# Optimization experiments

Measured on AMD Instinct MI355X. Metric: run time of the kernel, lower is better.

Reference implementation:

```python
import jax, jax.numpy as jnp
import numpy as np

NQ = 8          # n_qubits
NC = 4          # n_cycles of the angle encoder
PI = np.float32(np.pi)
LAYER_QUBITS = [[0, 1, 2, 3, 4, 5, 6, 7], [1, 3, 5, 7]]  # active qubits per conv layer
FINAL_QUBITS = [3, 7]                                    # active after last pooling
CX = jnp.array([[1, 0, 0, 0], [0, 1, 0, 0], [0, 0, 0, 1], [0, 0, 1, 0]], jnp.complex64)


def apply1(psi, U, q):
    """Apply 1-qubit gate U ((2,2) shared or (B,2,2) batched) on qubit q. psi: (B,2,...,2)."""
    psi = jnp.moveaxis(psi, 1 + q, -1)
    if U.ndim == 3:
        psi = jnp.einsum('bij,b...j->b...i', U, psi)
    else:
        psi = jnp.einsum('ij,...j->...i', U, psi)
    return jnp.moveaxis(psi, -1, 1 + q)


def apply2(psi, U, q0, q1):
    """Apply 2-qubit gate U (4,4) on (q0,q1); q0 is the more-significant wire."""
    psi = jnp.moveaxis(psi, (1 + q0, 1 + q1), (-2, -1))
    sh = psi.shape
    psi = jnp.einsum('ij,...j->...i', U, psi.reshape(sh[:-2] + (4,)))
    return jnp.moveaxis(psi.reshape(sh), (-2, -1), (1 + q0, 1 + q1))


def rz_mat(t):
    return jnp.array([[jnp.exp(-0.5j * t), 0.0], [0.0, jnp.exp(0.5j * t)]]).astype(jnp.complex64)


def ry_mat(t):
    c, s = jnp.cos(t / 2), jnp.sin(t / 2)
    return jnp.array([[c, -s], [s, c]]).astype(jnp.complex64)


def crx_mat(t):
    c = jnp.cos(t / 2).astype(jnp.complex64)
    s = jnp.sin(t / 2).astype(jnp.complex64)
    M = jnp.eye(4, dtype=jnp.complex64)
    return M.at[2, 2].set(c).at[3, 3].set(c).at[2, 3].set(-1j * s).at[3, 2].set(-1j * s)


def u3_mat(t, p, l):
    c, s = jnp.cos(t / 2), jnp.sin(t / 2)
    return jnp.array([[c + 0j, -jnp.exp(1j * l) * s],
                      [jnp.exp(1j * p) * s, jnp.exp(1j * (p + l)) * c]]).astype(jnp.complex64)


def expz(psi, q):
    """<Z_q> = P(q=0) - P(q=1)."""
    p = psi.real ** 2 + psi.imag ** 2
    p = jnp.moveaxis(p, 1 + q, 1).reshape(p.shape[0], 2, -1).sum(-1)
    return p[:, 0] - p[:, 1]


def encode(x):
    """Angle-encoding circuit (circuit_builder): NC cycles of RY(x) + CNOT ring."""
    B = x.shape[0]
    psi = jnp.zeros((B, 2 ** NQ), jnp.complex64).at[:, 0].set(1.0).reshape((B,) + (2,) * NQ)
    for c in range(NC):
        ang = x[:, c * NQ:(c + 1) * NQ]
        cc, ss = jnp.cos(ang / 2), jnp.sin(ang / 2)
        for q in range(NQ):
            U = jnp.stack([jnp.stack([cc[:, q], -ss[:, q]], -1),
                           jnp.stack([ss[:, q], cc[:, q]], -1)], -2).astype(jnp.complex64)
            psi = apply1(psi, U, q)
        for q in range(NQ):
            psi = apply2(psi, CX, q, (q + 1) % NQ)
    return psi


def forward(x, rz_p, ry_p, ry2_p, crx_p, u3_p, u3b_p, W1, b1, W2, b2):
    psi0 = encode(x)
    psi1 = psi0  # deepcopy of encoded state for the second feature map
    for layer in range(2):
        aq = LAYER_QUBITS[layer]
        n = len(aq)
        RZp, RYp, RY2p = rz_mat(rz_p[layer]), ry_mat(ry_p[layer]), ry_mat(ry2_p[layer])
        RZm, RZpl = rz_mat(-PI / 2), rz_mat(PI / 2)
        # circuit 1: ZNOTY-style conv blocks, even pairs then odd pairs
        for parity in (0, 1):
            for i in range(parity, n - 1, 2):
                qc, qt = aq[i], aq[i + 1]
                psi0 = apply1(psi0, RZm, qt)
                psi0 = apply2(psi0, CX, qt, qc)
                psi0 = apply1(psi0, RZp, qc)
                psi0 = apply1(psi0, RYp, qt)
                psi0 = apply2(psi0, CX, qc, qt)
                psi0 = apply1(psi0, RY2p, qt)
                psi0 = apply2(psi0, CX, qt, qc)
                psi0 = apply1(psi0, RZpl, qc)
        remain = [aq[i] for i in range(n) if i % 2 == 1]
        U3a = u3_mat(u3_p[layer, 0], u3_p[layer, 1], u3_p[layer, 2])
        for q in remain:
            psi0 = apply1(psi0, U3a, q)
        # circuit 2: CRX conv blocks, even pairs then odd pairs
        CRXp = crx_mat(crx_p[layer])
        for parity in (0, 1):
            for i in range(parity, n - 1, 2):
                psi1 = apply2(psi1, CRXp, aq[i], aq[i + 1])
        U3b = u3_mat(u3b_p[layer, 0], u3b_p[layer, 1], u3b_p[layer, 2])
        for q in remain:
            psi1 = apply1(psi1, U3b, q)
    xv = jnp.stack([expz(psi0, q) for q in FINAL_QUBITS], 1)  # (B,2)
    yv = jnp.stack([expz(psi1, q) for q in FINAL_QUBITS], 1)  # (B,2)
    feat = jnp.concatenate([xv, yv], 1)                       # (B,4)
    h = jnp.tanh(feat @ W1.T + b1)
    return jax.nn.sigmoid(h @ W2.T + b2)


def setup_inputs() -> dict:
    key = jax.random.key(0)
    ks = jax.random.split(key, 12)
    B = 8192
    return {
        'x': jax.random.normal(ks[0], (B, NC * NQ), jnp.float32),
        'rz_p': jax.random.normal(ks[1], (2,), jnp.float32) * 0.5,
        'ry_p': jax.random.normal(ks[2], (2,), jnp.float32) * 0.5,
        'ry2_p': jax.random.normal(ks[3], (2,), jnp.float32) * 0.5,
        'crx_p': jax.random.normal(ks[4], (2,), jnp.float32) * 0.5,
        'u3_p': jax.random.normal(ks[5], (2, 3), jnp.float32) * 0.5,
        'u3b_p': jax.random.normal(ks[6], (2, 3), jnp.float32) * 0.5,
        'W1': jax.random.normal(ks[7], (15, 4), jnp.float32) * 0.4,
        'b1': jax.random.normal(ks[8], (15,), jnp.float32) * 0.1,
        'W2': jax.random.normal(ks[9], (1, 15), jnp.float32) * 0.25,
        'b2': jax.random.normal(ks[10], (1,), jnp.float32) * 0.1,
    }


def reference(x, rz_p, ry_p, ry2_p, crx_p, u3_p, u3b_p, W1, b1, W2, b2):
    return forward(x, rz_p, ry_p, ry2_p, crx_p, u3_p, u3b_p, W1, b1, W2, b2)
```

## Files before the change

### kernel.cpp

```cpp
#include <hip/hip_runtime.h>

#define DEV __device__ __forceinline__


DEV int lpar(int lane, int m) { return __builtin_popcount(lane & m) & 1; }
constexpr int cpar(int v) { return (v ^ (v >> 1) ^ (v >> 2) ^ (v >> 3)) & 1; }

template<int LM, int SM, int LR, int SR>
DEV void ryr(float* p, float gc, float gs, int lane) {
  const float sg0 = lpar(lane, LR) ? gs : -gs;
  const float sg1 = -sg0;
  if constexpr (LM != 0) {
    float t[16];
    #pragma unroll
    for (int s = 0; s < 16; ++s) t[s] = __shfl_xor(p[s ^ SM], LM);
    #pragma unroll
    for (int s = 0; s < 16; ++s)
      p[s] = gc * p[s] + (cpar(s & SR) ? sg1 : sg0) * t[s];
  } else {
    constexpr int LOW = SM & (-SM);
    #pragma unroll
    for (int s = 0; s < 16; ++s) if (!(s & LOW)) {
      const int s1 = s ^ SM;
      float a = p[s], b = p[s1];
      float sg = cpar(s & SR) ? sg1 : sg0;
      p[s]  = gc * a + sg * b;
      p[s1] = gc * b - sg * a;
    }
  }
}

template<int LM, int SM, int LR, int SR>
DEV void u3_g(float* pr, float* pi, const float* u, int lane) {
  const bool hl = lpar(lane, LR);
  const float d0r = hl ? u[6] : u[0], d0i = hl ? u[7] : u[1];
  const float o0r = hl ? u[4] : u[2], o0i = hl ? u[5] : u[3];
  const float d1r = hl ? u[0] : u[6], d1i = hl ? u[1] : u[7];
  const float o1r = hl ? u[2] : u[4], o1i = hl ? u[3] : u[5];
  if constexpr (LM != 0) {
    float tr[16], ti[16];
    #pragma unroll
    for (int s = 0; s < 16; ++s) {
      tr[s] = __shfl_xor(pr[s ^ SM], LM);
      ti[s] = __shfl_xor(pi[s ^ SM], LM);
    }
    #pragma unroll
    for (int s = 0; s < 16; ++s) {
      const bool c1 = cpar(s & SR);
      const float dr = c1 ? d1r : d0r, di = c1 ? d1i : d0i;
      const float orr = c1 ? o1r : o0r, oi = c1 ? o1i : o0i;
      float ar = pr[s], ai = pi[s];
      pr[s] = dr*ar - di*ai + orr*tr[s] - oi*ti[s];
      pi[s] = dr*ai + di*ar + orr*ti[s] + oi*tr[s];
    }
  } else {
    constexpr int LOW = SM & (-SM);
    #pragma unroll
    for (int s = 0; s < 16; ++s) if (!(s & LOW)) {
      const int s1 = s ^ SM;
      const bool c1 = cpar(s & SR);
      const float dAr = c1 ? d1r : d0r, dAi = c1 ? d1i : d0i;
      const float oAr = c1 ? o1r : o0r, oAi = c1 ? o1i : o0i;
      const float dBr = c1 ? d0r : d1r, dBi = c1 ? d0i : d1i;
      const float oBr = c1 ? o0r : o1r, oBi = c1 ? o0i : o1i;
      float ar = pr[s], ai = pi[s], br = pr[s1], bi = pi[s1];
      pr[s]  = dAr*ar - dAi*ai + oAr*br - oAi*bi;
      pi[s]  = dAr*ai + dAi*ar + oAr*bi + oAi*br;
      pr[s1] = dBr*br - dBi*bi + oBr*ar - oBi*ai;
      pi[s1] = dBr*bi + dBi*br + oBr*ai + oBi*ar;
    }
  }
}

#define U4CLASS(Q)                                                            \
  if constexpr (!(((SRc == 0) && (Q & 2)) || ((SRt == 0) && (Q & 1)))) {      \
    const int r1 = R ^ Q, r2 = r1 ^ 2;                                        \
    const float2 wd = w2[r1 * 4 + r1],       wo = w2[r1 * 4 + (r1 ^ 1)];      \
    const float2 vd = w2[r2 * 4 + r1],       vo = w2[r2 * 4 + (r1 ^ 1)];      \
    _Pragma("unroll")                                                         \
    for (int s = 0; s < 16; ++s)                                              \
      if (((cpar(s & SRc) << 1) | cpar(s & SRt)) == Q) {                      \
        float ar = pr[s], ai = pi[s], br = tr[s], bi = ti[s];                 \
        pr[s] = wd.x*ar - wd.y*ai + wo.x*br - wo.y*bi;                        \
        pi[s] = wd.x*ai + wd.y*ar + wo.x*bi + wo.y*br;                        \
        tr[s] = vd.x*ar - vd.y*ai + vo.x*br - vo.y*bi;                        \
        ti[s] = vd.x*ai + vd.y*ar + vo.x*bi + vo.y*br;                        \
      }                                                                       \
  }

template<int LMc, int SMc, int LMt, int SMt, int LRc, int SRc, int LRt, int SRt>
DEV void u4_g(float* pr, float* pi, const float2* w2, int lane) {
  const int R = (lpar(lane, LRc) << 1) | lpar(lane, LRt);
  float tr[16], ti[16];
  #pragma unroll
  for (int s = 0; s < 16; ++s) {
    float vr = pr[s ^ SMt], vi = pi[s ^ SMt];
    if constexpr (LMt != 0) { vr = __shfl_xor(vr, LMt); vi = __shfl_xor(vi, LMt); }
    tr[s] = vr; ti[s] = vi;
  }
  U4CLASS(0) U4CLASS(1) U4CLASS(2) U4CLASS(3)
  #pragma unroll
  for (int s = 0; s < 16; ++s) {
    float br = tr[s ^ SMc], bi = ti[s ^ SMc];
    if constexpr (LMc != 0) { br = __shfl_xor(br, LMc); bi = __shfl_xor(bi, LMc); }
    pr[s] += br; pi[s] += bi;
  }
}

DEV void u3_make(float t, float p, float l, float* u) {
  float c = __cosf(0.5f * t), s = __sinf(0.5f * t);
  float cp = __cosf(p), sp = __sinf(p);
  float cl = __cosf(l), sl = __sinf(l);
  float cpl = __cosf(p + l), spl = __sinf(p + l);
  u[0] = c;        u[1] = 0.0f;
  u[2] = -cl * s;  u[3] = -sl * s;
  u[4] = cp * s;   u[5] = sp * s;
  u[6] = cpl * c;  u[7] = spl * c;
}

DEV void expz_fin(const float* pr, const float* pi, int lane, float& z3, float& z7) {
  float t3 = 0.0f, t7 = 0.0f;
  #pragma unroll
  for (int s = 0; s < 16; ++s) {
    float p = pr[s] * pr[s] + pi[s] * pi[s];
    t7 += p;
    t3 += (s & 1) ? -p : p;
  }
  if (lpar(lane, 10)) { t3 = -t3; t7 = -t7; }
  #pragma unroll
  for (int m = 1; m < 16; m <<= 1) {
    t3 += __shfl_xor(t3, m);
    t7 += __shfl_xor(t7, m);
  }
  z3 = t3; z7 = t7;
}


__global__ __launch_bounds__(256, 2)
void qcnn_kernel(const float* __restrict__ x,
                 const float* __restrict__ rz_p, const float* __restrict__ ry_p,
                 const float* __restrict__ ry2_p, const float* __restrict__ crx_p,
                 const float* __restrict__ u3_p, const float* __restrict__ u3b_p,
                 const float* __restrict__ W1, const float* __restrict__ b1,
                 const float* __restrict__ W2, const float* __restrict__ b2,
                 float* __restrict__ out, int B) {
  __shared__ __align__(8) float cw[128];

  const int tid  = threadIdx.x;
  const int lane = tid & 63;
  const int wave = tid >> 6;
  const int grp  = lane >> 4;
  const int sub  = lane & 15;
  const int st   = grp & 1;
  const int gb   = lane & 48;
  const int elem = blockIdx.x * 8 + wave * 2 + (grp >> 1);
  const int elemc = elem < B ? elem : (B - 1);

  if (tid < 32) {
    const int lay = tid >> 4, e = tid & 15, i4 = e >> 2, j4 = e & 3;
    const int base = tid & 48;
    const float c45 = 0.70710678118654752f;
    float rz = rz_p[lay], ry = ry_p[lay], ry2 = ry2_p[lay];
    float mr = (i4 == j4) ? c45 : 0.0f;
    float mi = (i4 == j4) ? ((i4 & 1) ? -c45 : c45) : 0.0f;
    { int t = (i4 & 1) ? (i4 ^ 2) : i4; int src = base | (t << 2) | j4;
      mr = __shfl(mr, src); mi = __shfl(mi, src); }
    { float cz = __cosf(0.5f * rz), sz = __sinf(0.5f * rz);
      float di = (i4 & 2) ? sz : -sz;
      float nr = cz * mr - di * mi, ni = cz * mi + di * mr; mr = nr; mi = ni; }
    { float cy = __cosf(0.5f * ry), sy = __sinf(0.5f * ry);
      int src = base | ((i4 ^ 1) << 2) | j4;
      float orr = __shfl(mr, src), oii = __shfl(mi, src);
      float sg = (i4 & 1) ? sy : -sy;
      mr = cy * mr + sg * orr; mi = cy * mi + sg * oii; }
    { int t = (i4 & 2) ? (i4 ^ 1) : i4; int src = base | (t << 2) | j4;
      mr = __shfl(mr, src); mi = __shfl(mi, src); }
    { float cy = __cosf(0.5f * ry2), sy = __sinf(0.5f * ry2);
      int src = base | ((i4 ^ 1) << 2) | j4;
      float orr = __shfl(mr, src), oii = __shfl(mi, src);
      float sg = (i4 & 1) ? sy : -sy;
      mr = cy * mr + sg * orr; mi = cy * mi + sg * oii; }
    { int t = (i4 & 1) ? (i4 ^ 2) : i4; int src = base | (t << 2) | j4;
      mr = __shfl(mr, src); mi = __shfl(mi, src); }
    { float di = (i4 & 2) ? c45 : -c45;
      float nr = c45 * mr - di * mi, ni = c45 * mi + di * mr; mr = nr; mi = ni; }
    cw[((lay * 2 + 0) * 16 + e) * 2]     = mr;
    cw[((lay * 2 + 0) * 16 + e) * 2 + 1] = mi;
  } else if (tid < 64) {
    const int t2 = tid - 32;
    const int lay = t2 >> 4, e = t2 & 15, i4 = e >> 2, j4 = e & 3;
    float t = crx_p[lay];
    float c = __cosf(0.5f * t), s = __sinf(0.5f * t);
    float mr = 0.0f, mi = 0.0f;
    if (i4 == j4) mr = (i4 < 2) ? 1.0f : c;
    if ((i4 >= 2) && ((i4 ^ j4) == 1)) mi = -s;
    cw[((lay * 2 + 1) * 16 + e) * 2]     = mr;
    cw[((lay * 2 + 1) * 16 + e) * 2 + 1] = mi;
  }

  float2 aa = ((const float2*)x)[(size_t)elemc * 16 + sub];
  float ch0 = __cosf(0.5f * aa.x), sh0 = __sinf(0.5f * aa.x);
  float ch1 = __cosf(0.5f * aa.y), sh1 = __sinf(0.5f * aa.y);

  float cq[8], sq[8];
  #pragma unroll
  for (int q = 0; q < 8; ++q) {
    cq[q] = __shfl((q & 1) ? ch1 : ch0, gb | (q >> 1));
    sq[q] = __shfl((q & 1) ? sh1 : sh0, gb | (q >> 1));
  }

  float p[16];
  {
    float g = ((sub & 8) ? sq[0] : cq[0]) * ((sub & 4) ? sq[2] : cq[2]) *
              ((sub & 2) ? sq[4] : cq[4]) * ((sub & 1) ? sq[6] : cq[6]);
    float h13[4] = {cq[1]*cq[3], cq[1]*sq[3], sq[1]*cq[3], sq[1]*sq[3]};
    float h57[4] = {cq[5]*cq[7], cq[5]*sq[7], sq[5]*cq[7], sq[5]*sq[7]};
    #pragma unroll
    for (int i = 0; i < 4; ++i) h13[i] *= g;
    #pragma unroll
    for (int s = 0; s < 16; ++s) p[s] = h13[s >> 2] * h57[s & 3];
  }

  #define ENC(k, LM, SM, LR, SR) {                                  \
    float gc = __shfl(((k) & 1) ? ch1 : ch0, gb | ((k) >> 1));      \
    float gs = __shfl(((k) & 1) ? sh1 : sh0, gb | ((k) >> 1));      \
    ryr<LM, SM, LR, SR>(p, gc, gs, lane); }

  ENC(8,  8,8, 7,15)  ENC(9,  4,8, 8,8)   ENC(10, 4,4, 12,8)  ENC(11, 2,4, 12,12)
  ENC(12, 2,2, 14,12) ENC(13, 1,2, 14,14) ENC(14, 1,1, 15,14) ENC(15, 8,9, 15,15)
  ENC(16, 12,0, 8,15) ENC(17, 0,12, 15,7) ENC(18, 6,0, 3,15)  ENC(19, 0,6, 15,3)
  ENC(20, 3,0, 1,15)  ENC(21, 0,3, 15,1)  ENC(22, 9,8, 0,15)  ENC(23, 4,9, 15,0)
  ENC(24, 12,12, 2,10) ENC(25, 6,12, 7,8) ENC(26, 6,6, 4,7)   ENC(27, 3,6, 11,4)
  ENC(28, 3,3, 10,11)  ENC(29, 9,11, 5,10) ENC(30, 13,1, 5,5) ENC(31, 8,5, 10,5)
  #undef ENC

  float pi_[16];
  #pragma unroll
  for (int s = 0; s < 16; ++s) pi_[s] = 0.0f;

  __syncthreads();
  const float2* w0 = ((const float2*)cw) + (0 * 2 + st) * 16;
  const float2* w1 = ((const float2*)cw) + (1 * 2 + st) * 16;

  u4_g<10,0,  0,10, 8,10, 5,2 >(p, pi_, w0, lane);
  u4_g<5,0,   0,5,  1,5,  10,1>(p, pi_, w0, lane);
  u4_g<10,8,  4,10, 0,10, 5,0 >(p, pi_, w0, lane);
  u4_g<5,4,   2,5,  0,5,  10,0>(p, pi_, w0, lane);
  u4_g<0,10,  5,0,  5,2,  1,5 >(p, pi_, w0, lane);
  u4_g<0,5,   10,8, 10,1, 0,10>(p, pi_, w0, lane);
  u4_g<4,10,  5,4,  5,0,  0,5 >(p, pi_, w0, lane);
  {
    float ua[8], ub[8], us[8];
    u3_make(u3_p[0], u3_p[1], u3_p[2], ua);
    u3_make(u3b_p[0], u3b_p[1], u3b_p[2], ub);
    #pragma unroll
    for (int k = 0; k < 8; ++k) us[k] = st ? ub[k] : ua[k];
    u3_g<0,10, 5,2 >(p, pi_, us, lane);
    u3_g<0,5,  10,1>(p, pi_, us, lane);
    u3_g<4,10, 5,0 >(p, pi_, us, lane);
    u3_g<2,5,  10,0>(p, pi_, us, lane);
  }
  u4_g<0,10,  0,5,  5,2,  10,1>(p, pi_, w1, lane);
  u4_g<4,10,  2,5,  5,0,  10,0>(p, pi_, w1, lane);
  u4_g<0,5,   4,10, 10,1, 5,0 >(p, pi_, w1, lane);
  {
    float ua[8], ub[8], us[8];
    u3_make(u3_p[3], u3_p[4], u3_p[5], ua);
    u3_make(u3b_p[3], u3b_p[4], u3b_p[5], ub);
    #pragma unroll
    for (int k = 0; k < 8; ++k) us[k] = st ? ub[k] : ua[k];
    u3_g<0,5,  10,1>(p, pi_, us, lane);
    u3_g<2,5,  10,0>(p, pi_, us, lane);
  }

  float z3, z7;
  expz_fin(p, pi_, lane, z3, z7);
  float o3 = __shfl_xor(z3, 16);
  float o7 = __shfl_xor(z7, 16);
  const float f0 = st ? o3 : z3, f1 = st ? o7 : z7;
  const float f2 = st ? z3 : o3, f3 = st ? z7 : o7;

  const int j = (sub < 15) ? sub : 0;
  float acc = W1[j * 4 + 0] * f0 + W1[j * 4 + 1] * f1 +
              W1[j * 4 + 2] * f2 + W1[j * 4 + 3] * f3 + b1[j];
  float e2 = __expf(2.0f * acc);
  float th = (e2 - 1.0f) / (e2 + 1.0f);
  float part = (sub < 15) ? th * W2[j] : 0.0f;
  #pragma unroll
  for (int m = 1; m < 16; m <<= 1) part += __shfl_xor(part, m);

  if (sub == 0 && st == 0 && elem < B) {
    float z = part + b2[0];
    out[elem] = 1.0f / (1.0f + __expf(-z));
  }
}

extern "C" void kernel_launch(void* const* d_in, const int* in_sizes, int n_in,
                              void* d_out, int out_size, void* d_ws, size_t ws_size,
                              hipStream_t stream) {
  (void)n_in; (void)out_size; (void)d_ws; (void)ws_size;
  const float* x     = (const float*)d_in[0];
  const float* rz_p  = (const float*)d_in[1];
  const float* ry_p  = (const float*)d_in[2];
  const float* ry2_p = (const float*)d_in[3];
  const float* crx_p = (const float*)d_in[4];
  const float* u3_p  = (const float*)d_in[5];
  const float* u3b_p = (const float*)d_in[6];
  const float* W1    = (const float*)d_in[7];
  const float* b1    = (const float*)d_in[8];
  const float* W2    = (const float*)d_in[9];
  const float* b2    = (const float*)d_in[10];
  float* out = (float*)d_out;

  const int B = in_sizes[0] / 32;
  const int blocks = (B + 7) / 8;
  qcnn_kernel<<<dim3(blocks), dim3(256), 0, stream>>>(
      x, rz_p, ry_p, ry2_p, crx_p, u3_p, u3b_p, W1, b1, W2, b2, out, B);
}
```

Measured before the change: 136.4 us.

## Remap state to 32 lanes x 8 amplitudes, run two branches sequentially

Before, each batch element used 32 lanes (two 16-lane halves, one per circuit branch), each holding 16 amplitudes. Now each element uses 32 lanes holding 8 amplitudes each. The encoded state is computed once and the two conv branches run one after another in a loop that reuses it. This halves per-thread register arrays and drops the duplicated encoding work across branch halves, but doubles the serial branch computation and changes which operations become cross-lane shuffles.

```diff
diff --git a/kernel.cpp b/kernel.cpp
--- a/kernel.cpp
+++ b/kernel.cpp
@@ -4,26 +4,26 @@
 
 
 DEV int lpar(int lane, int m) { return __builtin_popcount(lane & m) & 1; }
-constexpr int cpar(int v) { return (v ^ (v >> 1) ^ (v >> 2) ^ (v >> 3)) & 1; }
+constexpr int cpar3(int v) { return (v ^ (v >> 1) ^ (v >> 2)) & 1; }
 
 template<int LM, int SM, int LR, int SR>
 DEV void ryr(float* p, float gc, float gs, int lane) {
   const float sg0 = lpar(lane, LR) ? gs : -gs;
   const float sg1 = -sg0;
   if constexpr (LM != 0) {
-    float t[16];
-    #pragma unroll
-    for (int s = 0; s < 16; ++s) t[s] = __shfl_xor(p[s ^ SM], LM);
-    #pragma unroll
-    for (int s = 0; s < 16; ++s)
-      p[s] = gc * p[s] + (cpar(s & SR) ? sg1 : sg0) * t[s];
+    float t[8];
+    #pragma unroll
+    for (int s = 0; s < 8; ++s) t[s] = __shfl_xor(p[s ^ SM], LM);
+    #pragma unroll
+    for (int s = 0; s < 8; ++s)
+      p[s] = gc * p[s] + (cpar3(s & SR) ? sg1 : sg0) * t[s];
   } else {
     constexpr int LOW = SM & (-SM);
     #pragma unroll
-    for (int s = 0; s < 16; ++s) if (!(s & LOW)) {
+    for (int s = 0; s < 8; ++s) if (!(s & LOW)) {
       const int s1 = s ^ SM;
       float a = p[s], b = p[s1];
-      float sg = cpar(s & SR) ? sg1 : sg0;
+      float sg = cpar3(s & SR) ? sg1 : sg0;
       p[s]  = gc * a + sg * b;
       p[s1] = gc * b - sg * a;
     }
@@ -38,15 +38,15 @@
   const float d1r = hl ? u[0] : u[6], d1i = hl ? u[1] : u[7];
   const float o1r = hl ? u[2] : u[4], o1i = hl ? u[3] : u[5];
   if constexpr (LM != 0) {
-    float tr[16], ti[16];
-    #pragma unroll
-    for (int s = 0; s < 16; ++s) {
+    float tr[8], ti[8];
+    #pragma unroll
+    for (int s = 0; s < 8; ++s) {
       tr[s] = __shfl_xor(pr[s ^ SM], LM);
       ti[s] = __shfl_xor(pi[s ^ SM], LM);
     }
     #pragma unroll
-    for (int s = 0; s < 16; ++s) {
-      const bool c1 = cpar(s & SR);
+    for (int s = 0; s < 8; ++s) {
+      const bool c1 = cpar3(s & SR);
       const float dr = c1 ? d1r : d0r, di = c1 ? d1i : d0i;
       const float orr = c1 ? o1r : o0r, oi = c1 ? o1i : o0i;
       float ar = pr[s], ai = pi[s];
@@ -56,9 +56,9 @@
   } else {
     constexpr int LOW = SM & (-SM);
     #pragma unroll
-    for (int s = 0; s < 16; ++s) if (!(s & LOW)) {
+    for (int s = 0; s < 8; ++s) if (!(s & LOW)) {
       const int s1 = s ^ SM;
-      const bool c1 = cpar(s & SR);
+      const bool c1 = cpar3(s & SR);
       const float dAr = c1 ? d1r : d0r, dAi = c1 ? d1i : d0i;
       const float oAr = c1 ? o1r : o0r, oAi = c1 ? o1i : o0i;
       const float dBr = c1 ? d0r : d1r, dBi = c1 ? d0i : d1i;
@@ -78,8 +78,8 @@
     const float2 wd = w2[r1 * 4 + r1],       wo = w2[r1 * 4 + (r1 ^ 1)];      \
     const float2 vd = w2[r2 * 4 + r1],       vo = w2[r2 * 4 + (r1 ^ 1)];      \
     _Pragma("unroll")                                                         \
-    for (int s = 0; s < 16; ++s)                                              \
-      if (((cpar(s & SRc) << 1) | cpar(s & SRt)) == Q) {                      \
+    for (int s = 0; s < 8; ++s)                                               \
+      if (((cpar3(s & SRc) << 1) | cpar3(s & SRt)) == Q) {                    \
         float ar = pr[s], ai = pi[s], br = tr[s], bi = ti[s];                 \
         pr[s] = wd.x*ar - wd.y*ai + wo.x*br - wo.y*bi;                        \
         pi[s] = wd.x*ai + wd.y*ar + wo.x*bi + wo.y*br;                        \
@@ -91,16 +91,16 @@
 template<int LMc, int SMc, int LMt, int SMt, int LRc, int SRc, int LRt, int SRt>
 DEV void u4_g(float* pr, float* pi, const float2* w2, int lane) {
   const int R = (lpar(lane, LRc) << 1) | lpar(lane, LRt);
-  float tr[16], ti[16];
-  #pragma unroll
-  for (int s = 0; s < 16; ++s) {
+  float tr[8], ti[8];
+  #pragma unroll
+  for (int s = 0; s < 8; ++s) {
     float vr = pr[s ^ SMt], vi = pi[s ^ SMt];
     if constexpr (LMt != 0) { vr = __shfl_xor(vr, LMt); vi = __shfl_xor(vi, LMt); }
     tr[s] = vr; ti[s] = vi;
   }
   U4CLASS(0) U4CLASS(1) U4CLASS(2) U4CLASS(3)
   #pragma unroll
-  for (int s = 0; s < 16; ++s) {
+  for (int s = 0; s < 8; ++s) {
     float br = tr[s ^ SMc], bi = ti[s ^ SMc];
     if constexpr (LMc != 0) { br = __shfl_xor(br, LMc); bi = __shfl_xor(bi, LMc); }
     pr[s] += br; pi[s] += bi;
@@ -121,14 +121,14 @@
 DEV void expz_fin(const float* pr, const float* pi, int lane, float& z3, float& z7) {
   float t3 = 0.0f, t7 = 0.0f;
   #pragma unroll
-  for (int s = 0; s < 16; ++s) {
+  for (int s = 0; s < 8; ++s) {
     float p = pr[s] * pr[s] + pi[s] * pi[s];
     t7 += p;
     t3 += (s & 1) ? -p : p;
   }
-  if (lpar(lane, 10)) { t3 = -t3; t7 = -t7; }
-  #pragma unroll
-  for (int m = 1; m < 16; m <<= 1) {
+  if (lpar(lane, 20)) { t3 = -t3; t7 = -t7; }
+  #pragma unroll
+  for (int m = 1; m < 32; m <<= 1) {
     t3 += __shfl_xor(t3, m);
     t7 += __shfl_xor(t7, m);
   }
@@ -149,11 +149,9 @@
   const int tid  = threadIdx.x;
   const int lane = tid & 63;
   const int wave = tid >> 6;
-  const int grp  = lane >> 4;
-  const int sub  = lane & 15;
-  const int st   = grp & 1;
-  const int gb   = lane & 48;
-  const int elem = blockIdx.x * 8 + wave * 2 + (grp >> 1);
+  const int l5   = lane & 31;
+  const int hb   = lane & 32;
+  const int elem = blockIdx.x * 8 + wave * 2 + (lane >> 5);
   const int elemc = elem < B ? elem : (B - 1);
 
   if (tid < 32) {
@@ -198,98 +196,94 @@
     cw[((lay * 2 + 1) * 16 + e) * 2 + 1] = mi;
   }
 
-  float2 aa = ((const float2*)x)[(size_t)elemc * 16 + sub];
-  float ch0 = __cosf(0.5f * aa.x), sh0 = __sinf(0.5f * aa.x);
-  float ch1 = __cosf(0.5f * aa.y), sh1 = __sinf(0.5f * aa.y);
+  float a0 = x[(size_t)elemc * 32 + l5];
+  float ch = __cosf(0.5f * a0), sh = __sinf(0.5f * a0);
 
   float cq[8], sq[8];
   #pragma unroll
   for (int q = 0; q < 8; ++q) {
-    cq[q] = __shfl((q & 1) ? ch1 : ch0, gb | (q >> 1));
-    sq[q] = __shfl((q & 1) ? sh1 : sh0, gb | (q >> 1));
-  }
-
-  float p[16];
+    cq[q] = __shfl(ch, hb | q);
+    sq[q] = __shfl(sh, hb | q);
+  }
+
+  float p[8];
   {
-    float g = ((sub & 8) ? sq[0] : cq[0]) * ((sub & 4) ? sq[2] : cq[2]) *
-              ((sub & 2) ? sq[4] : cq[4]) * ((sub & 1) ? sq[6] : cq[6]);
-    float h13[4] = {cq[1]*cq[3], cq[1]*sq[3], sq[1]*cq[3], sq[1]*sq[3]};
-    float h57[4] = {cq[5]*cq[7], cq[5]*sq[7], sq[5]*cq[7], sq[5]*sq[7]};
-    #pragma unroll
-    for (int i = 0; i < 4; ++i) h13[i] *= g;
-    #pragma unroll
-    for (int s = 0; s < 16; ++s) p[s] = h13[s >> 2] * h57[s & 3];
-  }
-
-  #define ENC(k, LM, SM, LR, SR) {                                  \
-    float gc = __shfl(((k) & 1) ? ch1 : ch0, gb | ((k) >> 1));      \
-    float gs = __shfl(((k) & 1) ? sh1 : sh0, gb | ((k) >> 1));      \
+    float g = ((l5 & 16) ? sq[0] : cq[0]) * ((l5 & 8) ? sq[2] : cq[2]) *
+              ((l5 & 4)  ? sq[4] : cq[4]) * ((l5 & 2) ? sq[6] : cq[6]) *
+              ((l5 & 1)  ? sq[1] : cq[1]);
+    #pragma unroll
+    for (int s = 0; s < 8; ++s)
+      p[s] = g * ((s & 4) ? sq[3] : cq[3]) * ((s & 2) ? sq[5] : cq[5]) *
+                 ((s & 1) ? sq[7] : cq[7]);
+  }
+
+  #define ENC(k, LM, SM, LR, SR) {                 \
+    float gc = __shfl(ch, hb | (k));               \
+    float gs = __shfl(sh, hb | (k));               \
     ryr<LM, SM, LR, SR>(p, gc, gs, lane); }
 
-  ENC(8,  8,8, 7,15)  ENC(9,  4,8, 8,8)   ENC(10, 4,4, 12,8)  ENC(11, 2,4, 12,12)
-  ENC(12, 2,2, 14,12) ENC(13, 1,2, 14,14) ENC(14, 1,1, 15,14) ENC(15, 8,9, 15,15)
-  ENC(16, 12,0, 8,15) ENC(17, 0,12, 15,7) ENC(18, 6,0, 3,15)  ENC(19, 0,6, 15,3)
-  ENC(20, 3,0, 1,15)  ENC(21, 0,3, 15,1)  ENC(22, 9,8, 0,15)  ENC(23, 4,9, 15,0)
-  ENC(24, 12,12, 2,10) ENC(25, 6,12, 7,8) ENC(26, 6,6, 4,7)   ENC(27, 3,6, 11,4)
-  ENC(28, 3,3, 10,11)  ENC(29, 9,11, 5,10) ENC(30, 13,1, 5,5) ENC(31, 8,5, 10,5)
+  ENC(8,  17,0, 15,7)  ENC(9,  9,0,  17,0)  ENC(10, 8,4,  25,0)  ENC(11, 4,4,  25,4)
+  ENC(12, 4,2,  29,4)  ENC(13, 2,2,  29,6)  ENC(14, 2,1,  31,6)  ENC(15, 17,1, 31,7)
+  ENC(16, 24,0, 17,7)  ENC(17, 1,4,  30,7)  ENC(18, 12,0, 7,7)   ENC(19, 0,6,  30,3)
+  ENC(20, 6,0,  3,7)   ENC(21, 0,3,  30,1)  ENC(22, 19,0, 1,7)   ENC(23, 9,1,  30,0)
+  ENC(24, 25,4, 5,2)   ENC(25, 13,4, 15,0)  ENC(26, 12,6, 8,7)   ENC(27, 6,6,  22,4)
+  ENC(28, 6,3,  21,3)  ENC(29, 19,3, 11,2)  ENC(30, 26,1, 10,5)  ENC(31, 16,5, 20,5)
   #undef ENC
 
-  float pi_[16];
-  #pragma unroll
-  for (int s = 0; s < 16; ++s) pi_[s] = 0.0f;
+  float enc[8];
+  #pragma unroll
+  for (int s = 0; s < 8; ++s) enc[s] = p[s];
 
   __syncthreads();
-  const float2* w0 = ((const float2*)cw) + (0 * 2 + st) * 16;
-  const float2* w1 = ((const float2*)cw) + (1 * 2 + st) * 16;
-
-  u4_g<10,0,  0,10, 8,10, 5,2 >(p, pi_, w0, lane);
-  u4_g<5,0,   0,5,  1,5,  10,1>(p, pi_, w0, lane);
-  u4_g<10,8,  4,10, 0,10, 5,0 >(p, pi_, w0, lane);
-  u4_g<5,4,   2,5,  0,5,  10,0>(p, pi_, w0, lane);
-  u4_g<0,10,  5,0,  5,2,  1,5 >(p, pi_, w0, lane);
-  u4_g<0,5,   10,8, 10,1, 0,10>(p, pi_, w0, lane);
-  u4_g<4,10,  5,4,  5,0,  0,5 >(p, pi_, w0, lane);
-  {
-    float ua[8], ub[8], us[8];
-    u3_make(u3_p[0], u3_p[1], u3_p[2], ua);
-    u3_make(u3b_p[0], u3b_p[1], u3b_p[2], ub);
-    #pragma unroll
-    for (int k = 0; k < 8; ++k) us[k] = st ? ub[k] : ua[k];
-    u3_g<0,10, 5,2 >(p, pi_, us, lane);
-    u3_g<0,5,  10,1>(p, pi_, us, lane);
-    u3_g<4,10, 5,0 >(p, pi_, us, lane);
-    u3_g<2,5,  10,0>(p, pi_, us, lane);
-  }
-  u4_g<0,10,  0,5,  5,2,  10,1>(p, pi_, w1, lane);
-  u4_g<4,10,  2,5,  5,0,  10,0>(p, pi_, w1, lane);
-  u4_g<0,5,   4,10, 10,1, 5,0 >(p, pi_, w1, lane);
-  {
-    float ua[8], ub[8], us[8];
-    u3_make(u3_p[3], u3_p[4], u3_p[5], ua);
-    u3_make(u3b_p[3], u3b_p[4], u3b_p[5], ub);
-    #pragma unroll
-    for (int k = 0; k < 8; ++k) us[k] = st ? ub[k] : ua[k];
-    u3_g<0,5,  10,1>(p, pi_, us, lane);
-    u3_g<2,5,  10,0>(p, pi_, us, lane);
-  }
-
-  float z3, z7;
-  expz_fin(p, pi_, lane, z3, z7);
-  float o3 = __shfl_xor(z3, 16);
-  float o7 = __shfl_xor(z7, 16);
-  const float f0 = st ? o3 : z3, f1 = st ? o7 : z7;
-  const float f2 = st ? z3 : o3, f3 = st ? z7 : o7;
-
-  const int j = (sub < 15) ? sub : 0;
-  float acc = W1[j * 4 + 0] * f0 + W1[j * 4 + 1] * f1 +
-              W1[j * 4 + 2] * f2 + W1[j * 4 + 3] * f3 + b1[j];
+
+  float fz3[2], fz7[2];
+
+  #pragma unroll 1
+  for (int it = 0; it < 2; ++it) {
+    const float2* wL0 = ((const float2*)cw) + (0 * 2 + it) * 16;
+    const float2* wL1 = ((const float2*)cw) + (1 * 2 + it) * 16;
+    const float* u3src = it ? u3b_p : u3_p;
+
+    float pi_[8];
+    #pragma unroll
+    for (int s = 0; s < 8; ++s) { p[s] = enc[s]; pi_[s] = 0.0f; }
+
+    u4_g<20,0, 1,2,  17,2, 10,2>(p, pi_, wL0, lane);
+    u4_g<10,0, 0,5,  2,5,  20,1>(p, pi_, wL0, lane);
+    u4_g<21,0, 9,2,  1,2,  10,0>(p, pi_, wL0, lane);
+    u4_g<10,4, 4,5,  0,5,  20,0>(p, pi_, wL0, lane);
+    u4_g<1,2,  10,0, 10,2, 2,5 >(p, pi_, wL0, lane);
+    u4_g<0,5,  21,0, 20,1, 1,2 >(p, pi_, wL0, lane);
+    u4_g<9,2,  10,4, 10,0, 0,5 >(p, pi_, wL0, lane);
+    {
+      float us[8]; u3_make(u3src[0], u3src[1], u3src[2], us);
+      u3_g<1,2, 10,2>(p, pi_, us, lane);
+      u3_g<0,5, 20,1>(p, pi_, us, lane);
+      u3_g<9,2, 10,0>(p, pi_, us, lane);
+      u3_g<4,5, 20,0>(p, pi_, us, lane);
+    }
+    u4_g<1,2,  0,5,  10,2, 20,1>(p, pi_, wL1, lane);
+    u4_g<9,2,  4,5,  10,0, 20,0>(p, pi_, wL1, lane);
+    u4_g<0,5,  9,2,  20,1, 10,0>(p, pi_, wL1, lane);
+    {
+      float us[8]; u3_make(u3src[3], u3src[4], u3src[5], us);
+      u3_g<0,5, 20,1>(p, pi_, us, lane);
+      u3_g<4,5, 20,0>(p, pi_, us, lane);
+    }
+
+    expz_fin(p, pi_, lane, fz3[it], fz7[it]);
+  }
+
+  const int j = (l5 < 15) ? l5 : 0;
+  float acc = W1[j * 4 + 0] * fz3[0] + W1[j * 4 + 1] * fz7[0] +
+              W1[j * 4 + 2] * fz3[1] + W1[j * 4 + 3] * fz7[1] + b1[j];
   float e2 = __expf(2.0f * acc);
   float th = (e2 - 1.0f) / (e2 + 1.0f);
-  float part = (sub < 15) ? th * W2[j] : 0.0f;
-  #pragma unroll
-  for (int m = 1; m < 16; m <<= 1) part += __shfl_xor(part, m);
-
-  if (sub == 0 && st == 0 && elem < B) {
+  float part = (l5 < 15) ? th * W2[j] : 0.0f;
+  #pragma unroll
+  for (int m = 1; m < 32; m <<= 1) part += __shfl_xor(part, m);
+
+  if (l5 == 0 && elem < B) {
     float z = part + b2[0];
     out[elem] = 1.0f / (1.0f + __expf(-z));
   }
```

Result: faster. 132.9 us (-2.6%).
